# Kernel tuning notes

Measured on AMD Instinct MI355X. Metric: run time of the kernel, lower is better.

Reference implementation:

```python
import jax, jax.numpy as jnp
import numpy as np

B, T, C = 2, 2048, 2048
H = 16
D = C // H  # head_dim = 128


def setup_inputs() -> dict:
    key = jax.random.key(0)
    ks = jax.random.split(key, 7)
    scale = C ** -0.5
    x = jax.random.normal(ks[0], (B, T, C), dtype=jnp.float32)
    padding_mask = jax.random.randint(ks[1], (B, T), 0, 2, dtype=jnp.int32)
    Wq = jax.random.normal(ks[2], (C, C), dtype=jnp.float32) * scale
    Wk = jax.random.normal(ks[3], (C, C), dtype=jnp.float32) * scale
    Wv = jax.random.normal(ks[4], (C, C), dtype=jnp.float32) * scale
    Wp = jax.random.normal(ks[5], (C, C), dtype=jnp.float32) * scale
    bp = jax.random.normal(ks[6], (C,), dtype=jnp.float32) * 0.01
    return {"x": x, "padding_mask": padding_mask, "Wq": Wq, "Wk": Wk,
            "Wv": Wv, "Wp": Wp, "bp": bp}


def reference(x, padding_mask, Wq, Wk, Wv, Wp, bp):
    b, t, c = x.shape
    # projections (nn.Linear: x @ W.T), split heads -> [B,H,T,D]
    q = (x @ Wq.T).reshape(b, t, H, D).transpose(0, 2, 1, 3)
    k = (x @ Wk.T).reshape(b, t, H, D).transpose(0, 2, 1, 3)
    v = (x @ Wv.T).reshape(b, t, H, D).transpose(0, 2, 1, 3)
    scores = jnp.einsum('bhtd,bhsd->bhts', q, k) * (D ** -0.5)  # [B,H,T,T]
    # padding mask broadcasts along query rows: pm[b,i] masks row i (as in torch source)
    scores = jnp.where(padding_mask[:, None, :, None] == 0, jnp.float32(-1e9), scores)
    # causal mask
    causal = jnp.tril(jnp.ones((t, t), dtype=bool))
    scores = jnp.where(causal, scores, -jnp.inf)
    attn = jax.nn.softmax(scores, axis=-1)
    ctx = jnp.einsum('bhts,bhsd->bhtd', attn, v)
    ctx = ctx.transpose(0, 2, 1, 3).reshape(b, t, c)
    return ctx @ Wp.T + bp
```

## Files before the change

### kernel.cpp

```cpp
#include <hip/hip_runtime.h>
#include <stdint.h>

typedef __attribute__((ext_vector_type(8))) short vshort8;
typedef __attribute__((ext_vector_type(4))) short vshort4;
typedef __attribute__((ext_vector_type(4))) float vfloat4;

__device__ __forceinline__ short f2bf(float f) {
  union { float f; uint32_t u; } v; v.f = f;
  uint32_t r = (v.u + 0x7FFFu + ((v.u >> 16) & 1u)) >> 16;
  return (short)r;
}
__device__ __forceinline__ void gl_lds16(const void* g, void* l) {
  __builtin_amdgcn_global_load_lds(
      (const __attribute__((address_space(1))) void*)g,
      (__attribute__((address_space(3))) void*)l, 16, 0, 0);
}

__global__ void cvt_kernel(const float* __restrict__ src, short* __restrict__ dst,
                           int n) {
  int i = (blockIdx.x * blockDim.x + threadIdx.x) * 8;
  if (i >= n) return;
  vfloat4 a = *(const vfloat4*)(src + i);
  vfloat4 b = *(const vfloat4*)(src + i + 4);
  vshort8 o;
#pragma unroll
  for (int j = 0; j < 4; ++j) { o[j] = f2bf(a[j]); o[j + 4] = f2bf(b[j]); }
  *(vshort8*)(dst + i) = o;
}

__global__ void cvt3_kernel(const float* __restrict__ s0, const float* __restrict__ s1,
                            const float* __restrict__ s2, short* __restrict__ dst, int n) {
  const float* s = (blockIdx.y == 0) ? s0 : ((blockIdx.y == 1) ? s1 : s2);
  int i = (blockIdx.x * blockDim.x + threadIdx.x) * 8;
  if (i >= n) return;
  vfloat4 a = *(const vfloat4*)(s + i);
  vfloat4 b = *(const vfloat4*)(s + i + 4);
  vshort8 o;
#pragma unroll
  for (int j = 0; j < 4; ++j) { o[j] = f2bf(a[j]); o[j + 4] = f2bf(b[j]); }
  *(vshort8*)(dst + (size_t)blockIdx.y * n + i) = o;
}

#define GEMM_MAIN_LOOP()                                                        \
  const int tid  = threadIdx.x;                                                 \
  const int lane = tid & 63;                                                    \
  const int w    = tid >> 6;                                                    \
  const int wr   = w >> 2;                                                      \
  const int wc   = w & 3;                                                       \
  const int lrow = lane & 15;                                                   \
  const int quad = lane >> 4;                                                   \
  const int swz  = lrow & 7;                                                    \
  const int m0   = blockIdx.y * 128;                                            \
  const int n0   = blockIdx.x * 256;                                            \
  const int rr   = tid >> 3;                                                    \
  const int cg8  = ((tid & 7) ^ ((tid >> 3) & 7)) * 8;                          \
  const short* Ag = Aptr + (size_t)(m0 + rr) * K + cg8;                         \
  const short* Bg = Bptr + (size_t)(n0 + rr) * K + cg8;                         \
  auto stageA = [&](int bb, int kt, int i) {                                    \
    gl_lds16(Ag + (size_t)i * 64 * K + (size_t)kt * 64,                         \
             (void*)&lds[bb][i * 4096 + tid * 8]);                              \
  };                                                                            \
  auto stageB = [&](int bb, int kt, int i) {                                    \
    gl_lds16(Bg + (size_t)i * 64 * K + (size_t)kt * 64,                         \
             (void*)&lds[bb][8192 + i * 4096 + tid * 8]);                       \
  };                                                                            \
  const int aoff = (wr * 64 + lrow) * 64;                                       \
  const int boff = (wc * 64 + lrow) * 64;                                       \
  const int g8a0 = (quad ^ swz) * 8;                                            \
  const int g8a1 = ((4 + quad) ^ swz) * 8;                                      \
  vfloat4 acc[4][4] = {};                                                       \
  const int NT = K >> 6;                                                        \
  stageA(0, 0, 0); stageA(0, 0, 1);                                             \
  stageB(0, 0, 0); stageB(0, 0, 1); stageB(0, 0, 2); stageB(0, 0, 3);           \
  stageA(1, 1, 0); stageA(1, 1, 1);                                             \
  stageB(1, 1, 0); stageB(1, 1, 1); stageB(1, 1, 2); stageB(1, 1, 3);           \
  int cbuf = 0;                                                                 \
  for (int t = 0; t < NT; ++t) {                                                \
    const short* As = lds[cbuf];                                                \
    const short* Bs = lds[cbuf] + 8192;                                         \
    const int sb = (cbuf == 0) ? 2 : cbuf - 1;            \
    if (t + 1 < NT) {                                                           \
      asm volatile("s_waitcnt vmcnt(6)" ::: "memory");                          \
    } else {                                                                    \
      asm volatile("s_waitcnt vmcnt(0)" ::: "memory");                          \
    }                                                                           \
    __builtin_amdgcn_s_barrier();                                               \
    __builtin_amdgcn_sched_barrier(0);                                          \
    if (t + 2 < NT) {                                                           \
      stageA(sb, t + 2, 0); stageA(sb, t + 2, 1);                               \
      stageB(sb, t + 2, 0); stageB(sb, t + 2, 1);                               \
      stageB(sb, t + 2, 2); stageB(sb, t + 2, 3);                               \
    }                                                                           \
    vshort8 a[4][2], b[4][2];                                                   \
    _Pragma("unroll") for (int i = 0; i < 4; ++i) {                             \
      a[i][0] = *(const vshort8*)(As + aoff + i * 1024 + g8a0);                 \
      a[i][1] = *(const vshort8*)(As + aoff + i * 1024 + g8a1);                 \
      b[i][0] = *(const vshort8*)(Bs + boff + i * 1024 + g8a0);                 \
      b[i][1] = *(const vshort8*)(Bs + boff + i * 1024 + g8a1);                 \
    }                                                                           \
    __builtin_amdgcn_s_setprio(1);                                              \
    _Pragma("unroll") for (int mi = 0; mi < 4; ++mi)                            \
      _Pragma("unroll") for (int ni = 0; ni < 4; ++ni)                          \
        _Pragma("unroll") for (int ks = 0; ks < 2; ++ks)                        \
          acc[mi][ni] = __builtin_amdgcn_mfma_f32_16x16x32_bf16(                \
              a[mi][ks], b[ni][ks], acc[mi][ni], 0, 0, 0);                      \
    __builtin_amdgcn_s_setprio(0);                                              \
    __builtin_amdgcn_sched_barrier(0);                                          \
    cbuf = (cbuf == 2) ? 0 : cbuf + 1;                                          \
  }

__global__ __launch_bounds__(512, 2) void gemm_qkv(
    const short* __restrict__ Aptr, const short* __restrict__ Bptr,
    short* __restrict__ Qw, short* __restrict__ Kw, short* __restrict__ Vtw,
    int M, int K, float scale) {
  __shared__ __attribute__((aligned(16))) short lds[3][24576];
  GEMM_MAIN_LOOP()

  const int region = n0 >> 11;
#pragma unroll
  for (int mi = 0; mi < 4; ++mi) {
    int mbase = m0 + wr * 64 + mi * 16 + quad * 4;
#pragma unroll
    for (int ni = 0; ni < 4; ++ni) {
      int ng = n0 + wc * 64 + ni * 16 + lrow;
      int nn = ng & 2047;
      if (region == 2) {
        vshort4 sv;
#pragma unroll
        for (int r = 0; r < 4; ++r) sv[r] = f2bf(acc[mi][ni][r]);
        *(vshort4*)(Vtw + (size_t)nn * 4096 + mbase) = sv;
      } else if (region == 0) {
#pragma unroll
        for (int r = 0; r < 4; ++r)
          Qw[(size_t)(mbase + r) * 2048 + nn] = f2bf(acc[mi][ni][r] * scale);
      } else {
#pragma unroll
        for (int r = 0; r < 4; ++r)
          Kw[(size_t)(mbase + r) * 2048 + nn] = f2bf(acc[mi][ni][r]);
      }
    }
  }
}

__global__ __launch_bounds__(512, 2) void gemm_proj(
    const short* __restrict__ Aptr, const short* __restrict__ Bptr,
    float* __restrict__ C, const float* __restrict__ bias,
    int M, int K, int ldC) {
  __shared__ __attribute__((aligned(16))) short lds[3][24576];
  GEMM_MAIN_LOOP()

#pragma unroll
  for (int mi = 0; mi < 4; ++mi) {
    int mbase = m0 + wr * 64 + mi * 16 + quad * 4;
#pragma unroll
    for (int ni = 0; ni < 4; ++ni) {
      int n = n0 + wc * 64 + ni * 16 + lrow;
      float badd = bias[n];
#pragma unroll
      for (int r = 0; r < 4; ++r)
        C[(size_t)(mbase + r) * ldC + n] = acc[mi][ni][r] + badd;
    }
  }
}

__global__ __launch_bounds__(256, 1) void attn_kernel(
    const short* __restrict__ Q, const short* __restrict__ Kg,
    const short* __restrict__ Vt, const int* __restrict__ pm,
    short* __restrict__ ctx) {
  const int T = 2048, Cd = 2048, D = 128, MT = 4096;
  __shared__ __attribute__((aligned(16))) short Kb[3][8192];
  __shared__ __attribute__((aligned(16))) short Vb[3][8192];
  __shared__ __attribute__((aligned(16))) short Ps[4][32][72];

  const int tid  = threadIdx.x;
  const int lane = tid & 63;
  const int w    = tid >> 6;
  const int lrow = lane & 15;
  const int quad = lane >> 4;
  const int pb = blockIdx.x, h = blockIdx.y, b = blockIdx.z;

  vshort8 ones;
#pragma unroll
  for (int i = 0; i < 8; ++i) ones[i] = (short)0x3F80;

  auto stage = [&](int bb, int j) {
#pragma unroll
    for (int i = 0; i < 4; ++i) {
      int s = i * 256 + tid;
      int kr = s >> 4, kg = s & 15;
      gl_lds16(Kg + (size_t)(b * T + j * 64 + kr) * Cd + h * D + (kg ^ (kr & 15)) * 8,
               (void*)&Kb[bb][s * 8]);
    }
#pragma unroll
    for (int i = 0; i < 4; ++i) {
      int s = i * 256 + tid;
      int vr = s >> 3, vg = s & 7;
      gl_lds16(Vt + (size_t)(h * D + vr) * MT + b * T + j * 64 + (vg ^ (vr & 7)) * 8,
               (void*)&Vb[bb][s * 8]);
    }
  };

#pragma unroll 1
  for (int tt = 0; tt < 2; ++tt) {
    const int qt = tt ? (15 - pb) : pb;
    const int q0 = qt * 128 + w * 32;
    const int jmax = 2 * qt + 1;

    vshort8 qf[2][4];
#pragma unroll
    for (int mi = 0; mi < 2; ++mi)
#pragma unroll
      for (int ks = 0; ks < 4; ++ks)
        qf[mi][ks] = *(const vshort8*)(Q + (size_t)(b * T + q0 + mi * 16 + lrow) * Cd +
                                       h * D + ks * 32 + quad * 8);
    bool keep[2][4];
#pragma unroll
    for (int mi = 0; mi < 2; ++mi)
#pragma unroll
      for (int r = 0; r < 4; ++r)
        keep[mi][r] = pm[b * T + q0 + mi * 16 + quad * 4 + r] != 0;

    vfloat4 oacc[2][8] = {};
    vfloat4 osum[2] = {};

    __builtin_amdgcn_s_barrier();
    stage(0, 0);
    stage(1, 1);

#pragma unroll 1
    for (int j = 0; j <= jmax; ++j) {
      if (j < jmax) {
        asm volatile("s_waitcnt vmcnt(8)" ::: "memory");
      } else {
        asm volatile("s_waitcnt vmcnt(0)" ::: "memory");
      }
      __builtin_amdgcn_s_barrier();
      __builtin_amdgcn_sched_barrier(0);
      if (j + 2 <= jmax) stage((j + 2) % 3, j + 2);

      const short* Ks_ = Kb[j % 3];
      const short* Vs_ = Vb[j % 3];

      vfloat4 sacc[2][4] = {};
#pragma unroll
      for (int nt = 0; nt < 4; ++nt) {
        vshort8 kf[4];
#pragma unroll
        for (int ks = 0; ks < 4; ++ks)
          kf[ks] = *(const vshort8*)(Ks_ + (nt * 16 + lrow) * 128 +
                                     ((ks * 4 + quad) ^ lrow) * 8);
#pragma unroll
        for (int mi = 0; mi < 2; ++mi)
#pragma unroll
          for (int ks = 0; ks < 4; ++ks)
            sacc[mi][nt] = __builtin_amdgcn_mfma_f32_16x16x32_bf16(
                qf[mi][ks], kf[ks], sacc[mi][nt], 0, 0, 0);
      }

#pragma unroll
      for (int mi = 0; mi < 2; ++mi)
#pragma unroll
        for (int nt = 0; nt < 4; ++nt) {
          int s_idx = j * 64 + nt * 16 + lrow;
#pragma unroll
          for (int r = 0; r < 4; ++r) {
            int qr = q0 + mi * 16 + quad * 4 + r;
            float sv = keep[mi][r] ? sacc[mi][nt][r] : 0.0f;
            float pe = __expf(sv - 12.0f);
            pe = (s_idx <= qr) ? pe : 0.0f;
            Ps[w][mi * 16 + quad * 4 + r][nt * 16 + lrow] = f2bf(pe);
          }
        }

      vshort8 pf[2][2];
#pragma unroll
      for (int mi = 0; mi < 2; ++mi)
#pragma unroll
        for (int kp = 0; kp < 2; ++kp)
          pf[mi][kp] = *(const vshort8*)(&Ps[w][mi * 16 + lrow][kp * 32 + quad * 8]);

#pragma unroll
      for (int mi = 0; mi < 2; ++mi)
#pragma unroll
        for (int kp = 0; kp < 2; ++kp)
          osum[mi] = __builtin_amdgcn_mfma_f32_16x16x32_bf16(pf[mi][kp], ones, osum[mi], 0, 0, 0);

#pragma unroll
      for (int dt = 0; dt < 8; ++dt) {
        vshort8 vf0 = *(const vshort8*)(Vs_ + (dt * 16 + lrow) * 64 +
                                        (quad ^ (lrow & 7)) * 8);
        vshort8 vf1 = *(const vshort8*)(Vs_ + (dt * 16 + lrow) * 64 +
                                        ((4 + quad) ^ (lrow & 7)) * 8);
#pragma unroll
        for (int mi = 0; mi < 2; ++mi) {
          oacc[mi][dt] = __builtin_amdgcn_mfma_f32_16x16x32_bf16(pf[mi][0], vf0, oacc[mi][dt], 0, 0, 0);
          oacc[mi][dt] = __builtin_amdgcn_mfma_f32_16x16x32_bf16(pf[mi][1], vf1, oacc[mi][dt], 0, 0, 0);
        }
      }
    }

#pragma unroll
    for (int mi = 0; mi < 2; ++mi) {
      float il[4];
#pragma unroll
      for (int r = 0; r < 4; ++r)
        il[r] = __builtin_amdgcn_rcpf(fmaxf(osum[mi][r], 1e-30f));
#pragma unroll
      for (int dt = 0; dt < 8; ++dt) {
        int d = dt * 16 + lrow;
#pragma unroll
        for (int r = 0; r < 4; ++r) {
          float o = oacc[mi][dt][r] * il[r];
          ctx[(size_t)(b * T + q0 + mi * 16 + quad * 4 + r) * Cd + h * D + d] = f2bf(o);
        }
      }
    }
  }
}

extern "C" void kernel_launch(void* const* d_in, const int* in_sizes, int n_in,
                              void* d_out, int out_size, void* d_ws, size_t ws_size,
                              hipStream_t stream) {
  (void)in_sizes; (void)n_in; (void)out_size; (void)ws_size;
  const float* x  = (const float*)d_in[0];
  const int*   pm = (const int*)d_in[1];
  const float* Wq = (const float*)d_in[2];
  const float* Wk = (const float*)d_in[3];
  const float* Wv = (const float*)d_in[4];
  const float* Wp = (const float*)d_in[5];
  const float* bp = (const float*)d_in[6];
  float* out = (float*)d_out;

  const int Bb = 2, T = 2048, Cd = 2048, M = Bb * T;
  const size_t SZ = (size_t)M * Cd;
  const size_t WZ = (size_t)Cd * Cd;
  short* xb   = (short*)d_ws;
  short* Qw   = xb + SZ;
  short* Kw   = Qw + SZ;
  short* Vtw  = Kw + SZ;
  short* Cx   = Vtw + SZ;
  short* wcat = Cx + SZ;

  const int CB = 256;
  dim3 gx(((int)SZ / 8 + CB - 1) / CB);
  dim3 gw(((int)WZ / 8 + CB - 1) / CB);
  const float scale = 0.08838834764831845f;

  cvt_kernel<<<gx, CB, 0, stream>>>(x, xb, (int)SZ);
  cvt3_kernel<<<dim3(gw.x, 3), CB, 0, stream>>>(Wq, Wk, Wv, wcat, (int)WZ);

  gemm_qkv<<<dim3(6144 / 256, M / 128), 512, 0, stream>>>(
      xb, wcat, Qw, Kw, Vtw, M, Cd, scale);

  attn_kernel<<<dim3(8, 16, Bb), 256, 0, stream>>>(Qw, Kw, Vtw, pm, Cx);

  cvt_kernel<<<gw, CB, 0, stream>>>(Wp, wcat, (int)WZ);
  gemm_proj<<<dim3(Cd / 256, M / 128), 512, 0, stream>>>(Cx, wcat, out, bp, M, Cd, Cd);
}
```

Measured before the change: 368.5 us.

## Software-pipeline QK^T one tile ahead in attention and merge conversion launches

The attention loop now computes the QK^T scores for the next KV tile while the softmax and PV of the current tile run. The shared-memory ring grows from three to four buffers so the early prefetch does not overwrite a tile still in use. Separately, the x and Wq/Wk/Wv fp32-to-bf16 conversions are merged into one launch, and Wp is converted into the now-unused xb buffer before attention. This trims launch overhead, at the cost of more shared memory and more live registers (the snext scores) in the attention kernel.

```diff
diff --git a/kernel.cpp b/kernel.cpp
--- a/kernel.cpp
+++ b/kernel.cpp
@@ -28,9 +28,13 @@
   *(vshort8*)(dst + i) = o;
 }
 
-__global__ void cvt3_kernel(const float* __restrict__ s0, const float* __restrict__ s1,
-                            const float* __restrict__ s2, short* __restrict__ dst, int n) {
-  const float* s = (blockIdx.y == 0) ? s0 : ((blockIdx.y == 1) ? s1 : s2);
+__global__ void cvt4_kernel(const float* __restrict__ s0, const float* __restrict__ s1,
+                            const float* __restrict__ s2, const float* __restrict__ s3,
+                            short* __restrict__ d0, short* __restrict__ d1,
+                            int n0, int n1) {
+  const int y = blockIdx.y;
+  const float* s = (y == 0) ? s0 : ((y == 1) ? s1 : ((y == 2) ? s2 : s3));
+  const int n = (y == 0) ? n0 : n1;
   int i = (blockIdx.x * blockDim.x + threadIdx.x) * 8;
   if (i >= n) return;
   vfloat4 a = *(const vfloat4*)(s + i);
@@ -38,7 +42,8 @@
   vshort8 o;
 #pragma unroll
   for (int j = 0; j < 4; ++j) { o[j] = f2bf(a[j]); o[j + 4] = f2bf(b[j]); }
-  *(vshort8*)(dst + (size_t)blockIdx.y * n + i) = o;
+  short* d = (y == 0) ? d0 : (d1 + (size_t)(y - 1) * n1);
+  *(vshort8*)(d + i) = o;
 }
 
 #define GEMM_MAIN_LOOP()                                                        \
@@ -168,8 +173,8 @@
     const short* __restrict__ Vt, const int* __restrict__ pm,
     short* __restrict__ ctx) {
   const int T = 2048, Cd = 2048, D = 128, MT = 4096;
-  __shared__ __attribute__((aligned(16))) short Kb[3][8192];
-  __shared__ __attribute__((aligned(16))) short Vb[3][8192];
+  __shared__ __attribute__((aligned(16))) short Kb[4][8192];
+  __shared__ __attribute__((aligned(16))) short Vb[4][8192];
   __shared__ __attribute__((aligned(16))) short Ps[4][32][72];
 
   const int tid  = threadIdx.x;
@@ -223,39 +228,47 @@
     vfloat4 oacc[2][8] = {};
     vfloat4 osum[2] = {};
 
+    auto qk = [&](int jj, vfloat4 (&sa)[2][4]) {
+      const short* Ks_ = Kb[jj & 3];
+#pragma unroll
+      for (int nt = 0; nt < 4; ++nt) {
+        vshort8 kf[4];
+#pragma unroll
+        for (int ks = 0; ks < 4; ++ks)
+          kf[ks] = *(const vshort8*)(Ks_ + (nt * 16 + lrow) * 128 +
+                                     ((ks * 4 + quad) ^ lrow) * 8);
+#pragma unroll
+        for (int mi = 0; mi < 2; ++mi)
+#pragma unroll
+          for (int ks = 0; ks < 4; ++ks)
+            sa[mi][nt] = __builtin_amdgcn_mfma_f32_16x16x32_bf16(
+                qf[mi][ks], kf[ks], sa[mi][nt], 0, 0, 0);
+      }
+    };
+
     __builtin_amdgcn_s_barrier();
     stage(0, 0);
     stage(1, 1);
+    asm volatile("s_waitcnt vmcnt(8)" ::: "memory");
+    __builtin_amdgcn_s_barrier();
+    __builtin_amdgcn_sched_barrier(0);
+
+    vfloat4 scur[2][4] = {};
+    qk(0, scur);
 
 #pragma unroll 1
     for (int j = 0; j <= jmax; ++j) {
-      if (j < jmax) {
+      if (j + 2 <= jmax) {
+        stage((j + 2) & 3, j + 2);
         asm volatile("s_waitcnt vmcnt(8)" ::: "memory");
-      } else {
+      } else if (j < jmax) {
         asm volatile("s_waitcnt vmcnt(0)" ::: "memory");
       }
       __builtin_amdgcn_s_barrier();
       __builtin_amdgcn_sched_barrier(0);
-      if (j + 2 <= jmax) stage((j + 2) % 3, j + 2);
-
-      const short* Ks_ = Kb[j % 3];
-      const short* Vs_ = Vb[j % 3];
-
-      vfloat4 sacc[2][4] = {};
-#pragma unroll
-      for (int nt = 0; nt < 4; ++nt) {
-        vshort8 kf[4];
-#pragma unroll
-        for (int ks = 0; ks < 4; ++ks)
-          kf[ks] = *(const vshort8*)(Ks_ + (nt * 16 + lrow) * 128 +
-                                     ((ks * 4 + quad) ^ lrow) * 8);
-#pragma unroll
-        for (int mi = 0; mi < 2; ++mi)
-#pragma unroll
-          for (int ks = 0; ks < 4; ++ks)
-            sacc[mi][nt] = __builtin_amdgcn_mfma_f32_16x16x32_bf16(
-                qf[mi][ks], kf[ks], sacc[mi][nt], 0, 0, 0);
-      }
+
+      vfloat4 snext[2][4] = {};
+      if (j < jmax) qk(j + 1, snext);
 
 #pragma unroll
       for (int mi = 0; mi < 2; ++mi)
@@ -265,7 +278,7 @@
 #pragma unroll
           for (int r = 0; r < 4; ++r) {
             int qr = q0 + mi * 16 + quad * 4 + r;
-            float sv = keep[mi][r] ? sacc[mi][nt][r] : 0.0f;
+            float sv = keep[mi][r] ? scur[mi][nt][r] : 0.0f;
             float pe = __expf(sv - 12.0f);
             pe = (s_idx <= qr) ? pe : 0.0f;
             Ps[w][mi * 16 + quad * 4 + r][nt * 16 + lrow] = f2bf(pe);
@@ -285,6 +298,7 @@
         for (int kp = 0; kp < 2; ++kp)
           osum[mi] = __builtin_amdgcn_mfma_f32_16x16x32_bf16(pf[mi][kp], ones, osum[mi], 0, 0, 0);
 
+      const short* Vs_ = Vb[j & 3];
 #pragma unroll
       for (int dt = 0; dt < 8; ++dt) {
         vshort8 vf0 = *(const vshort8*)(Vs_ + (dt * 16 + lrow) * 64 +
@@ -296,6 +310,14 @@
           oacc[mi][dt] = __builtin_amdgcn_mfma_f32_16x16x32_bf16(pf[mi][0], vf0, oacc[mi][dt], 0, 0, 0);
           oacc[mi][dt] = __builtin_amdgcn_mfma_f32_16x16x32_bf16(pf[mi][1], vf1, oacc[mi][dt], 0, 0, 0);
         }
+      }
+
+      if (j < jmax) {
+#pragma unroll
+        for (int mi = 0; mi < 2; ++mi)
+#pragma unroll
+          for (int nt = 0; nt < 4; ++nt)
+            scur[mi][nt] = snext[mi][nt];
       }
     }
 
@@ -342,18 +364,18 @@
   short* wcat = Cx + SZ;
 
   const int CB = 256;
-  dim3 gx(((int)SZ / 8 + CB - 1) / CB);
   dim3 gw(((int)WZ / 8 + CB - 1) / CB);
   const float scale = 0.08838834764831845f;
 
-  cvt_kernel<<<gx, CB, 0, stream>>>(x, xb, (int)SZ);
-  cvt3_kernel<<<dim3(gw.x, 3), CB, 0, stream>>>(Wq, Wk, Wv, wcat, (int)WZ);
+  cvt4_kernel<<<dim3(((int)SZ / 8 + CB - 1) / CB, 4), CB, 0, stream>>>(
+      x, Wq, Wk, Wv, xb, wcat, (int)SZ, (int)WZ);
 
   gemm_qkv<<<dim3(6144 / 256, M / 128), 512, 0, stream>>>(
       xb, wcat, Qw, Kw, Vtw, M, Cd, scale);
 
+  cvt_kernel<<<gw, CB, 0, stream>>>(Wp, xb, (int)WZ);
+
   attn_kernel<<<dim3(8, 16, Bb), 256, 0, stream>>>(Qw, Kw, Vtw, pm, Cx);
 
-  cvt_kernel<<<gw, CB, 0, stream>>>(Wp, wcat, (int)WZ);
-  gemm_proj<<<dim3(Cd / 256, M / 128), 512, 0, stream>>>(Cx, wcat, out, bp, M, Cd, Cd);
-}
+  gemm_proj<<<dim3(Cd / 256, M / 128), 512, 0, stream>>>(Cx, xb, out, bp, M, Cd, Cd);
+}
```

Result: no change. 374.9 us (+1.8%).

## Widen attention blocks to 512 threads with shared K/V tiles and merge conversions

Applied to the files above, without the earlier changes.

The attention kernel now has 8 waves per block, each covering a 256-row query tile, instead of 4 waves that process two 128-row tiles (one light, one heavy) in sequence. Each staged K/V tile is shared by twice as many waves, and waves skip key tiles past their causal limit. This removes the per-tile reload of Q and the restart of the pipeline, but the load becomes uneven across blocks since the paired-tile balancing is gone. The P scratch buffer gets an XOR swizzle to cut LDS bank conflicts, and the x/Wq/Wk/Wv conversions are merged into one launch, with the Wp conversion reusing the x buffer.

```diff
diff --git a/kernel.cpp b/kernel.cpp
--- a/kernel.cpp
+++ b/kernel.cpp
@@ -28,9 +28,13 @@
   *(vshort8*)(dst + i) = o;
 }
 
-__global__ void cvt3_kernel(const float* __restrict__ s0, const float* __restrict__ s1,
-                            const float* __restrict__ s2, short* __restrict__ dst, int n) {
-  const float* s = (blockIdx.y == 0) ? s0 : ((blockIdx.y == 1) ? s1 : s2);
+__global__ void cvt4_kernel(const float* __restrict__ s0, const float* __restrict__ s1,
+                            const float* __restrict__ s2, const float* __restrict__ s3,
+                            short* __restrict__ d0, short* __restrict__ d1,
+                            int n0, int n1) {
+  const int y = blockIdx.y;
+  const float* s = (y == 0) ? s0 : ((y == 1) ? s1 : ((y == 2) ? s2 : s3));
+  const int n = (y == 0) ? n0 : n1;
   int i = (blockIdx.x * blockDim.x + threadIdx.x) * 8;
   if (i >= n) return;
   vfloat4 a = *(const vfloat4*)(s + i);
@@ -38,7 +42,8 @@
   vshort8 o;
 #pragma unroll
   for (int j = 0; j < 4; ++j) { o[j] = f2bf(a[j]); o[j + 4] = f2bf(b[j]); }
-  *(vshort8*)(dst + (size_t)blockIdx.y * n + i) = o;
+  short* d = (y == 0) ? d0 : (d1 + (size_t)(y - 1) * n1);
+  *(vshort8*)(d + i) = o;
 }
 
 #define GEMM_MAIN_LOOP()                                                        \
@@ -163,21 +168,24 @@
   }
 }
 
-__global__ __launch_bounds__(256, 1) void attn_kernel(
+__global__ __launch_bounds__(512, 1) void attn_kernel(
     const short* __restrict__ Q, const short* __restrict__ Kg,
     const short* __restrict__ Vt, const int* __restrict__ pm,
     short* __restrict__ ctx) {
   const int T = 2048, Cd = 2048, D = 128, MT = 4096;
   __shared__ __attribute__((aligned(16))) short Kb[3][8192];
   __shared__ __attribute__((aligned(16))) short Vb[3][8192];
-  __shared__ __attribute__((aligned(16))) short Ps[4][32][72];
+  __shared__ __attribute__((aligned(16))) short Ps[8][2048];
 
   const int tid  = threadIdx.x;
   const int lane = tid & 63;
   const int w    = tid >> 6;
   const int lrow = lane & 15;
   const int quad = lane >> 4;
-  const int pb = blockIdx.x, h = blockIdx.y, b = blockIdx.z;
+  const int qt = blockIdx.x, h = blockIdx.y, b = blockIdx.z;
+  const int q0 = qt * 256 + w * 32;
+  const int jmax = 4 * qt + 3;
+  const int jw   = 4 * qt + (w >> 1);
 
   vshort8 ones;
 #pragma unroll
@@ -185,59 +193,53 @@
 
   auto stage = [&](int bb, int j) {
 #pragma unroll
-    for (int i = 0; i < 4; ++i) {
-      int s = i * 256 + tid;
+    for (int i = 0; i < 2; ++i) {
+      int s = i * 512 + tid;
       int kr = s >> 4, kg = s & 15;
       gl_lds16(Kg + (size_t)(b * T + j * 64 + kr) * Cd + h * D + (kg ^ (kr & 15)) * 8,
                (void*)&Kb[bb][s * 8]);
     }
 #pragma unroll
-    for (int i = 0; i < 4; ++i) {
-      int s = i * 256 + tid;
+    for (int i = 0; i < 2; ++i) {
+      int s = i * 512 + tid;
       int vr = s >> 3, vg = s & 7;
       gl_lds16(Vt + (size_t)(h * D + vr) * MT + b * T + j * 64 + (vg ^ (vr & 7)) * 8,
                (void*)&Vb[bb][s * 8]);
     }
   };
 
+  vshort8 qf[2][4];
+#pragma unroll
+  for (int mi = 0; mi < 2; ++mi)
+#pragma unroll
+    for (int ks = 0; ks < 4; ++ks)
+      qf[mi][ks] = *(const vshort8*)(Q + (size_t)(b * T + q0 + mi * 16 + lrow) * Cd +
+                                     h * D + ks * 32 + quad * 8);
+  bool keep[2][4];
+#pragma unroll
+  for (int mi = 0; mi < 2; ++mi)
+#pragma unroll
+    for (int r = 0; r < 4; ++r)
+      keep[mi][r] = pm[b * T + q0 + mi * 16 + quad * 4 + r] != 0;
+
+  vfloat4 oacc[2][8] = {};
+  vfloat4 osum[2] = {};
+
+  stage(0, 0);
+  stage(1, 1);
+
 #pragma unroll 1
-  for (int tt = 0; tt < 2; ++tt) {
-    const int qt = tt ? (15 - pb) : pb;
-    const int q0 = qt * 128 + w * 32;
-    const int jmax = 2 * qt + 1;
-
-    vshort8 qf[2][4];
-#pragma unroll
-    for (int mi = 0; mi < 2; ++mi)
-#pragma unroll
-      for (int ks = 0; ks < 4; ++ks)
-        qf[mi][ks] = *(const vshort8*)(Q + (size_t)(b * T + q0 + mi * 16 + lrow) * Cd +
-                                       h * D + ks * 32 + quad * 8);
-    bool keep[2][4];
-#pragma unroll
-    for (int mi = 0; mi < 2; ++mi)
-#pragma unroll
-      for (int r = 0; r < 4; ++r)
-        keep[mi][r] = pm[b * T + q0 + mi * 16 + quad * 4 + r] != 0;
-
-    vfloat4 oacc[2][8] = {};
-    vfloat4 osum[2] = {};
-
+  for (int j = 0; j <= jmax; ++j) {
+    if (j < jmax) {
+      asm volatile("s_waitcnt vmcnt(4)" ::: "memory");
+    } else {
+      asm volatile("s_waitcnt vmcnt(0)" ::: "memory");
+    }
     __builtin_amdgcn_s_barrier();
-    stage(0, 0);
-    stage(1, 1);
-
-#pragma unroll 1
-    for (int j = 0; j <= jmax; ++j) {
-      if (j < jmax) {
-        asm volatile("s_waitcnt vmcnt(8)" ::: "memory");
-      } else {
-        asm volatile("s_waitcnt vmcnt(0)" ::: "memory");
-      }
-      __builtin_amdgcn_s_barrier();
-      __builtin_amdgcn_sched_barrier(0);
-      if (j + 2 <= jmax) stage((j + 2) % 3, j + 2);
-
+    __builtin_amdgcn_sched_barrier(0);
+    if (j + 2 <= jmax) stage((j + 2) % 3, j + 2);
+
+    if (j <= jw) {
       const short* Ks_ = Kb[j % 3];
       const short* Vs_ = Vb[j % 3];
 
@@ -264,11 +266,13 @@
           int s_idx = j * 64 + nt * 16 + lrow;
 #pragma unroll
           for (int r = 0; r < 4; ++r) {
-            int qr = q0 + mi * 16 + quad * 4 + r;
+            int row_w = mi * 16 + quad * 4 + r;
+            int qr = q0 + row_w;
             float sv = keep[mi][r] ? sacc[mi][nt][r] : 0.0f;
             float pe = __expf(sv - 12.0f);
             pe = (s_idx <= qr) ? pe : 0.0f;
-            Ps[w][mi * 16 + quad * 4 + r][nt * 16 + lrow] = f2bf(pe);
+            int grp = (nt * 2 + (lrow >> 3)) ^ (row_w & 7);
+            Ps[w][row_w * 64 + grp * 8 + (lrow & 7)] = f2bf(pe);
           }
         }
 
@@ -277,7 +281,8 @@
       for (int mi = 0; mi < 2; ++mi)
 #pragma unroll
         for (int kp = 0; kp < 2; ++kp)
-          pf[mi][kp] = *(const vshort8*)(&Ps[w][mi * 16 + lrow][kp * 32 + quad * 8]);
+          pf[mi][kp] = *(const vshort8*)(&Ps[w][(mi * 16 + lrow) * 64 +
+                                               (((kp * 4 + quad) ^ (lrow & 7)) * 8)]);
 
 #pragma unroll
       for (int mi = 0; mi < 2; ++mi)
@@ -298,21 +303,21 @@
         }
       }
     }
-
-#pragma unroll
-    for (int mi = 0; mi < 2; ++mi) {
-      float il[4];
-#pragma unroll
-      for (int r = 0; r < 4; ++r)
-        il[r] = __builtin_amdgcn_rcpf(fmaxf(osum[mi][r], 1e-30f));
-#pragma unroll
-      for (int dt = 0; dt < 8; ++dt) {
-        int d = dt * 16 + lrow;
-#pragma unroll
-        for (int r = 0; r < 4; ++r) {
-          float o = oacc[mi][dt][r] * il[r];
-          ctx[(size_t)(b * T + q0 + mi * 16 + quad * 4 + r) * Cd + h * D + d] = f2bf(o);
-        }
+  }
+
+#pragma unroll
+  for (int mi = 0; mi < 2; ++mi) {
+    float il[4];
+#pragma unroll
+    for (int r = 0; r < 4; ++r)
+      il[r] = __builtin_amdgcn_rcpf(fmaxf(osum[mi][r], 1e-30f));
+#pragma unroll
+    for (int dt = 0; dt < 8; ++dt) {
+      int d = dt * 16 + lrow;
+#pragma unroll
+      for (int r = 0; r < 4; ++r) {
+        float o = oacc[mi][dt][r] * il[r];
+        ctx[(size_t)(b * T + q0 + mi * 16 + quad * 4 + r) * Cd + h * D + d] = f2bf(o);
       }
     }
   }
@@ -342,18 +347,18 @@
   short* wcat = Cx + SZ;
 
   const int CB = 256;
-  dim3 gx(((int)SZ / 8 + CB - 1) / CB);
   dim3 gw(((int)WZ / 8 + CB - 1) / CB);
   const float scale = 0.08838834764831845f;
 
-  cvt_kernel<<<gx, CB, 0, stream>>>(x, xb, (int)SZ);
-  cvt3_kernel<<<dim3(gw.x, 3), CB, 0, stream>>>(Wq, Wk, Wv, wcat, (int)WZ);
+  cvt4_kernel<<<dim3(((int)SZ / 8 + CB - 1) / CB, 4), CB, 0, stream>>>(
+      x, Wq, Wk, Wv, xb, wcat, (int)SZ, (int)WZ);
 
   gemm_qkv<<<dim3(6144 / 256, M / 128), 512, 0, stream>>>(
       xb, wcat, Qw, Kw, Vtw, M, Cd, scale);
 
-  attn_kernel<<<dim3(8, 16, Bb), 256, 0, stream>>>(Qw, Kw, Vtw, pm, Cx);
-
-  cvt_kernel<<<gw, CB, 0, stream>>>(Wp, wcat, (int)WZ);
-  gemm_proj<<<dim3(Cd / 256, M / 128), 512, 0, stream>>>(Cx, wcat, out, bp, M, Cd, Cd);
-}
+  cvt_kernel<<<gw, CB, 0, stream>>>(Wp, xb, (int)WZ);
+
+  attn_kernel<<<dim3(8, 16, Bb), 512, 0, stream>>>(Qw, Kw, Vtw, pm, Cx);
+
+  gemm_proj<<<dim3(Cd / 256, M / 128), 512, 0, stream>>>(Cx, xb, out, bp, M, Cd, Cd);
+}
```

Measured after the change: 377.2 us. 2.4% more time.
